# Optimization experiments

Hardware: AMD Instinct MI355X
Metric: run time of the kernel (lower is better)

The kernel has to match this reference:

```python
import jax, jax.numpy as jnp
import numpy as np

EMB = 256
HEADS = 4
HEAD_DIM = EMB // HEADS
N = 4096
M = 4096


def setup_inputs() -> dict:
    key = jax.random.key(0)
    ks = jax.random.split(key, 7)
    s = 1.0 / np.sqrt(EMB)  # keep logits in a sane range
    return {
        "A": jax.random.normal(ks[0], (N, EMB), jnp.float32),
        "B": jax.random.normal(ks[1], (M, EMB), jnp.float32),
        "Wq": jax.random.normal(ks[2], (EMB, EMB), jnp.float32) * s,
        "Wk": jax.random.normal(ks[3], (EMB, EMB), jnp.float32) * s,
        "Wv": jax.random.normal(ks[4], (EMB, EMB), jnp.float32) * s,
        "Wo": jax.random.normal(ks[5], (EMB, EMB), jnp.float32) * s,
        "bo": jnp.zeros((EMB,), jnp.float32),
    }


def _cross_attend(X, Y, Wq, Wk, Wv, Wo, bo):
    # X attends to Y. X:[n,emb], Y:[m,emb]
    scale = jnp.asarray(np.sqrt(HEAD_DIM), X.dtype)
    Q = (X @ Wq.T).reshape(X.shape[0], HEADS, HEAD_DIM)  # [n,h,d]
    K = (Y @ Wk.T).reshape(Y.shape[0], HEADS, HEAD_DIM)  # [m,h,d]
    V = (Y @ Wv.T).reshape(Y.shape[0], HEADS, HEAD_DIM)  # [m,h,d]
    scores = jnp.einsum("nhd,mhd->hnm", Q, K) / scale      # [h,n,m]
    attn = jax.nn.softmax(scores, axis=-1)                   # dropout p=0.0 -> identity
    ctx = jnp.einsum("hnm,mhd->nhd", attn, V).reshape(X.shape[0], EMB)
    return ctx @ Wo.T + bo + X                               # out proj + residual


def reference(A, B, Wq, Wk, Wv, Wo, bo):
    A_out = _cross_attend(A, B, Wq, Wk, Wv, Wo, bo)
    B_out = _cross_attend(B, A, Wq, Wk, Wv, Wo, bo)
    return (A_out, B_out)
```

## Files before the change

### kernel.cpp

```cpp
#include <hip/hip_runtime.h>
#include <hip/hip_bf16.h>
#include <math.h>

#define EMB 256
#define HEADS 4
#define HD 64
#define NTOK 4096

typedef __attribute__((ext_vector_type(8))) short bf16x8;
typedef __attribute__((ext_vector_type(4))) float f32x4;
typedef __attribute__((ext_vector_type(16))) float f32x16;

#define MFMA16(a, b, c) __builtin_amdgcn_mfma_f32_16x16x32_bf16(a, b, c, 0, 0, 0)
#define MFMA32(a, b, c) __builtin_amdgcn_mfma_f32_32x32x16_bf16(a, b, c, 0, 0, 0)

static __device__ __forceinline__ ushort f2bf(float f) {
    __hip_bfloat16 h = __float2bfloat16(f);
    return *(ushort*)&h;
}
static __device__ __forceinline__ float ex2(float x) { return __builtin_amdgcn_exp2f(x); }
static __device__ __forceinline__ uint pkbf(float lo, float hi) {
    uint r;
    asm("v_cvt_pk_bf16_f32 %0, %1, %2" : "=v"(r) : "v"(lo), "v"(hi));
    return r;
}
static __device__ __forceinline__ float max3f(float a, float b, float c) {
    float r;
    asm("v_max3_f32 %0, %1, %2, %3" : "=v"(r) : "v"(a), "v"(b), "v"(c));
    return r;
}
static __device__ __forceinline__ bf16x8 cvt8(float4 a, float4 b) {
    union { uint u[4]; bf16x8 h; } pk;
    pk.u[0] = pkbf(a.x, a.y);
    pk.u[1] = pkbf(a.z, a.w);
    pk.u[2] = pkbf(b.x, b.y);
    pk.u[3] = pkbf(b.z, b.w);
    return pk.h;
}
static __device__ __forceinline__ float bf2f(ushort u) {
    return __uint_as_float(((uint)u) << 16);
}

__global__ void cvtW(const float* __restrict__ Wq, const float* __restrict__ Wk,
                     const float* __restrict__ Wv, const float* __restrict__ Wo,
                     ushort* __restrict__ Wall) {
    const float* s = (blockIdx.y == 0) ? Wq : (blockIdx.y == 1) ? Wk : (blockIdx.y == 2) ? Wv : Wo;
    ushort* d = Wall + (size_t)blockIdx.y * 65536;
    int i = (blockIdx.x * 256 + threadIdx.x) * 4;
    float4 v = *(const float4*)(s + i);
    ushort4 o;
    o.x = f2bf(v.x); o.y = f2bf(v.y); o.z = f2bf(v.z); o.w = f2bf(v.w);
    *(ushort4*)(d + i) = o;
}

__global__ __launch_bounds__(256) void qkv_proj(const float* __restrict__ Xa,
                                                const float* __restrict__ Xb,
                                                const ushort* __restrict__ Wall,
                                                ushort* __restrict__ Q0, ushort* __restrict__ K1, ushort* __restrict__ Vt1,
                                                ushort* __restrict__ Q1, ushort* __restrict__ K0, ushort* __restrict__ Vt0) {
    int w = threadIdx.x >> 6, lane = threadIdx.x & 63;
    int lr = lane & 15, lg = lane >> 4;
    int z = blockIdx.z;
    const float* X = z ? Xb : Xa;
    ushort* Qo = z ? Q1 : Q0;
    ushort* Ko = z ? K0 : K1;
    ushort* Vto = z ? Vt0 : Vt1;
    int rbase = blockIdx.x * 64 + w * 16;
    int cbase = blockIdx.y * 64;

    f32x4 acc[3][4] = {};
#pragma unroll
    for (int kk = 0; kk < 256; kk += 32) {
        const float* xr = X + (size_t)(rbase + lr) * EMB + kk + lg * 8;
        bf16x8 a = cvt8(*(const float4*)xr, *(const float4*)(xr + 4));
#pragma unroll
        for (int kind = 0; kind < 3; ++kind) {
            const ushort* W = Wall + (size_t)kind * 65536;
#pragma unroll
            for (int cj = 0; cj < 4; ++cj) {
                bf16x8 b = *(const bf16x8*)(W + (size_t)(cbase + cj * 16 + lr) * EMB + kk + lg * 8);
                acc[kind][cj] = MFMA16(a, b, acc[kind][cj]);
            }
        }
    }
    const float QS = 0.125f * 1.4426950408889634f;
#pragma unroll
    for (int cj = 0; cj < 4; ++cj)
#pragma unroll
        for (int j = 0; j < 4; ++j) {
            int R = rbase + lg * 4 + j;
            int col = cbase + cj * 16 + lr;
            Qo[(size_t)R * EMB + col] = f2bf(acc[0][cj][j] * QS);
            Ko[(size_t)R * EMB + col] = f2bf(acc[1][cj][j]);
            int h = col >> 6, d = col & 63;
            int Rp = (R & ~12) | ((R & 4) << 1) | ((R & 8) >> 1);
            Vto[(size_t)h * HD * NTOK + (size_t)d * NTOK + Rp] = f2bf(acc[2][cj][j]);
        }
}

__global__ __launch_bounds__(256, 4) void attn(const ushort* __restrict__ Q0,
                                               const ushort* __restrict__ K0,
                                               const ushort* __restrict__ Vt0,
                                               const ushort* __restrict__ Q1,
                                               const ushort* __restrict__ K1,
                                               const ushort* __restrict__ Vt1,
                                               ushort* __restrict__ Opart,
                                               float* __restrict__ ML) {
    __shared__ ushort lK[2][64 * 64];
    __shared__ ushort lV[2][64 * 64];

    int fb = blockIdx.x + 32 * blockIdx.y + 128 * blockIdx.z;
    int nf = (fb & 7) * 128 + (fb >> 3);
    int qt = nf & 31;
    int head = (nf >> 5) & 3;
    int z = nf >> 7;
    int dir = z >> 2, split = z & 3;
    int kv0 = split * 1024;

    const ushort* Q = dir ? Q1 : Q0;
    const ushort* K = dir ? K1 : K0;
    const ushort* Vt = dir ? Vt1 : Vt0;
    const ushort* Vth = Vt + (size_t)head * HD * NTOK;

    int wq = threadIdx.x >> 6;
    int lane = threadIdx.x & 63;
    int l31 = lane & 31, hi = lane >> 5;

    int qg = qt * 128 + wq * 32 + l31;
    bf16x8 qf[4];
#pragma unroll
    for (int ks = 0; ks < 4; ++ks)
        qf[ks] = *(const bf16x8*)(Q + (size_t)qg * EMB + head * 64 + ks * 16 + hi * 8);

    int srow = threadIdx.x >> 3, sseg = threadIdx.x & 7;
    int ssw = (sseg ^ ((srow >> 2) & 7)) * 8;

    uint4 rk0 = *(const uint4*)(K + (size_t)(kv0 + srow) * EMB + head * 64 + sseg * 8);
    uint4 rk1 = *(const uint4*)(K + (size_t)(kv0 + srow + 32) * EMB + head * 64 + sseg * 8);
    uint4 rv0 = *(const uint4*)(Vth + (size_t)srow * NTOK + kv0 + sseg * 8);
    uint4 rv1 = *(const uint4*)(Vth + (size_t)(srow + 32) * NTOK + kv0 + sseg * 8);

    float m = -1e30f, ls = 0.0f;
    f32x16 oacc0 = {};
    f32x16 oacc1 = {};
    int sw = (l31 >> 2) & 7;

    for (int t = 0; t < 16; ++t) {
        int cur = t & 1;
        ushort* lk = &lK[cur][0];
        ushort* lv = &lV[cur][0];
        *(uint4*)(&lk[srow * 64 + ssw]) = rk0;
        *(uint4*)(&lk[(srow + 32) * 64 + ssw]) = rk1;
        *(uint4*)(&lv[srow * 64 + ssw]) = rv0;
        *(uint4*)(&lv[(srow + 32) * 64 + ssw]) = rv1;
        __syncthreads();

        if (t < 15) {
            int nkv = kv0 + (t + 1) * 64;
            rk0 = *(const uint4*)(K + (size_t)(nkv + srow) * EMB + head * 64 + sseg * 8);
            rk1 = *(const uint4*)(K + (size_t)(nkv + srow + 32) * EMB + head * 64 + sseg * 8);
            rv0 = *(const uint4*)(Vth + (size_t)srow * NTOK + nkv + sseg * 8);
            rv1 = *(const uint4*)(Vth + (size_t)(srow + 32) * NTOK + nkv + sseg * 8);
        }

        f32x16 sA = {}, sB = {};
        __builtin_amdgcn_s_setprio(1);
#pragma unroll
        for (int ks = 0; ks < 4; ++ks) {
            bf16x8 ka = *(const bf16x8*)(&lk[l31 * 64 + ((ks * 2 + hi) ^ sw) * 8]);
            bf16x8 kb = *(const bf16x8*)(&lk[(32 + l31) * 64 + ((ks * 2 + hi) ^ sw) * 8]);
            sA = MFMA32(ka, qf[ks], sA);
            sB = MFMA32(kb, qf[ks], sB);
        }
        __builtin_amdgcn_s_setprio(0);

        float t0 = max3f(sA[0], sA[1], sA[2]);
        float t1 = max3f(sA[3], sA[4], sA[5]);
        float t2 = max3f(sA[6], sA[7], sA[8]);
        float t3 = max3f(sA[9], sA[10], sA[11]);
        float t4 = max3f(sA[12], sA[13], sA[14]);
        float t5 = max3f(sB[0], sB[1], sB[2]);
        float t6 = max3f(sB[3], sB[4], sB[5]);
        float t7 = max3f(sB[6], sB[7], sB[8]);
        float t8 = max3f(sB[9], sB[10], sB[11]);
        float t9 = max3f(sB[12], sB[13], sB[14]);
        float ta = fmaxf(sA[15], sB[15]);
        float u0 = max3f(t0, t1, t2);
        float u1 = max3f(t3, t4, t5);
        float u2 = max3f(t6, t7, t8);
        float u3 = fmaxf(t9, ta);
        float tmax = fmaxf(max3f(u0, u1, u2), u3);
        tmax = fmaxf(tmax, __shfl_xor(tmax, 32));

        if (__any(tmax > m + 8.0f)) {
            float mn = fmaxf(m, tmax);
            float sc = ex2(m - mn);
            m = mn;
            ls *= sc;
#pragma unroll
            for (int r = 0; r < 16; ++r) { oacc0[r] *= sc; oacc1[r] *= sc; }
        }

#pragma unroll
        for (int r = 0; r < 16; ++r) sA[r] = ex2(sA[r] - m);
#pragma unroll
        for (int r = 0; r < 16; ++r) sB[r] = ex2(sB[r] - m);

        float s1[16];
#pragma unroll
        for (int i = 0; i < 8; ++i) s1[i] = sA[2 * i] + sA[2 * i + 1];
#pragma unroll
        for (int i = 0; i < 8; ++i) s1[8 + i] = sB[2 * i] + sB[2 * i + 1];
#pragma unroll
        for (int w2 = 8; w2 >= 1; w2 >>= 1)
#pragma unroll
            for (int i = 0; i < 8; ++i)
                if (i < w2) s1[i] = s1[2 * i] + s1[2 * i + 1];
        float rs = s1[0];
        rs += __shfl_xor(rs, 32);
        ls += rs;

        bf16x8 pa[4];
#pragma unroll
        for (int ks = 0; ks < 4; ++ks) {
            union { uint u[4]; bf16x8 h; } pk;
#pragma unroll
            for (int j = 0; j < 4; ++j) {
                float lo = (ks < 2) ? sA[(ks & 1) * 8 + 2 * j] : sB[(ks & 1) * 8 + 2 * j];
                float hv = (ks < 2) ? sA[(ks & 1) * 8 + 2 * j + 1] : sB[(ks & 1) * 8 + 2 * j + 1];
                pk.u[j] = pkbf(lo, hv);
            }
            pa[ks] = pk.h;
        }

        __builtin_amdgcn_s_setprio(1);
#pragma unroll
        for (int ks = 0; ks < 4; ++ks) {
            bf16x8 va = *(const bf16x8*)(&lv[l31 * 64 + ((ks * 2 + hi) ^ sw) * 8]);
            bf16x8 vb = *(const bf16x8*)(&lv[(32 + l31) * 64 + ((ks * 2 + hi) ^ sw) * 8]);
            oacc0 = MFMA32(va, pa[ks], oacc0);
            oacc1 = MFMA32(vb, pa[ks], oacc1);
        }
        __builtin_amdgcn_s_setprio(0);
    }

    ushort* Ob = Opart + ((size_t)z * 4096 + qg) * 256 + head * 64;
#pragma unroll
    for (int r = 0; r < 16; ++r) {
        int crow = (r & 3) + 8 * (r >> 2) + 4 * hi;
        Ob[crow] = f2bf(oacc0[r]);
        Ob[32 + crow] = f2bf(oacc1[r]);
    }
    if (hi == 0) {
        float2* mlp = (float2*)ML;
        mlp[((size_t)z * 4 + head) * 4096 + qg] = make_float2(m, ls);
    }
}

__global__ __launch_bounds__(256) void merge(const ushort* __restrict__ Opart,
                                             const float* __restrict__ ML,
                                             ushort* __restrict__ C0,
                                             ushort* __restrict__ C1) {
    int idx = blockIdx.x * 256 + threadIdx.x;
    int dblk = idx & 7;
    int head = (idx >> 3) & 3;
    int q = (idx >> 5) & 4095;
    int dir = idx >> 17;

    const float2* mlp = (const float2*)ML;
    float2 ml[4];
    float M = -1e30f;
#pragma unroll
    for (int s = 0; s < 4; ++s) {
        ml[s] = mlp[((size_t)(dir * 4 + s) * 4 + head) * 4096 + q];
        M = fmaxf(M, ml[s].x);
    }
    float denom = 0.0f, a[4];
#pragma unroll
    for (int s = 0; s < 4; ++s) { a[s] = ex2(ml[s].x - M); denom += a[s] * ml[s].y; }
    float inv = 1.0f / denom;

    float accv[8] = {};
#pragma unroll
    for (int s = 0; s < 4; ++s) {
        float ws = a[s] * inv;
        bf16x8 x = *(const bf16x8*)(Opart + ((size_t)(dir * 4 + s) * 4096 + q) * 256 + head * 64 + dblk * 8);
#pragma unroll
        for (int u = 0; u < 8; ++u) accv[u] += ws * bf2f((ushort)x[u]);
    }
    float4 c0 = {accv[0], accv[1], accv[2], accv[3]};
    float4 c1 = {accv[4], accv[5], accv[6], accv[7]};
    ushort* C = (dir ? C1 : C0) + (size_t)q * 256 + head * 64 + dblk * 8;
    *(bf16x8*)C = cvt8(c0, c1);
}

__global__ __launch_bounds__(256) void out_proj(const ushort* __restrict__ C0,
                                                const ushort* __restrict__ C1,
                                                const ushort* __restrict__ Wo,
                                                const float* __restrict__ bo,
                                                const float* __restrict__ A,
                                                const float* __restrict__ B,
                                                float* __restrict__ out) {
    int dir = blockIdx.z;
    const ushort* Ctx = dir ? C1 : C0;
    const float* X = dir ? B : A;
    float* o = out + (size_t)dir * NTOK * EMB;

    int w = threadIdx.x >> 6, lane = threadIdx.x & 63;
    int lr = lane & 15, lg = lane >> 4;
    int rbase = blockIdx.x * 64 + w * 16;
    int cbase = blockIdx.y * 64;

    f32x4 acc[4] = {};
#pragma unroll
    for (int kk = 0; kk < 256; kk += 32) {
        bf16x8 a = *(const bf16x8*)(Ctx + (size_t)(rbase + lr) * EMB + kk + lg * 8);
#pragma unroll
        for (int cj = 0; cj < 4; ++cj) {
            bf16x8 b = *(const bf16x8*)(Wo + (size_t)(cbase + cj * 16 + lr) * EMB + kk + lg * 8);
            acc[cj] = MFMA16(a, b, acc[cj]);
        }
    }
#pragma unroll
    for (int cj = 0; cj < 4; ++cj)
#pragma unroll
        for (int j = 0; j < 4; ++j) {
            int R = rbase + lg * 4 + j;
            int col = cbase + cj * 16 + lr;
            o[(size_t)R * EMB + col] = acc[cj][j] + bo[col] + X[(size_t)R * EMB + col];
        }
}

extern "C" void kernel_launch(void* const* d_in, const int* in_sizes, int n_in,
                              void* d_out, int out_size, void* d_ws, size_t ws_size,
                              hipStream_t stream) {
    const float* A  = (const float*)d_in[0];
    const float* B  = (const float*)d_in[1];
    const float* Wq = (const float*)d_in[2];
    const float* Wk = (const float*)d_in[3];
    const float* Wv = (const float*)d_in[4];
    const float* Wo = (const float*)d_in[5];
    const float* bo = (const float*)d_in[6];
    float* out = (float*)d_out;

    ushort* ws = (ushort*)d_ws;
    const size_t TE = (size_t)NTOK * EMB;
    ushort* wall = ws;
    ushort* q0  = wall + 4 * 65536;
    ushort* q1  = q0 + TE;
    ushort* k0  = q1 + TE;
    ushort* k1  = k0 + TE;
    ushort* vt0 = k1 + TE;
    ushort* vt1 = vt0 + TE;
    ushort* c0  = vt1 + TE;
    ushort* c1  = c0 + TE;
    ushort* Opart = c1 + TE;
    float* ML = (float*)(Opart + (size_t)8 * 4096 * 256);

    cvtW<<<dim3(64, 4), 256, 0, stream>>>(Wq, Wk, Wv, Wo, wall);

    qkv_proj<<<dim3(64, 4, 2), 256, 0, stream>>>(A, B, wall, q0, k1, vt1, q1, k0, vt0);

    attn<<<dim3(32, 4, 8), 256, 0, stream>>>(q0, k0, vt0, q1, k1, vt1, Opart, ML);

    merge<<<dim3(1024), 256, 0, stream>>>(Opart, ML, c0, c1);

    out_proj<<<dim3(64, 4, 2), 256, 0, stream>>>(c0, c1, wall + 3 * 65536, bo, A, B, out);
}
```

Measured before the change: 105.8 us.

## Pre-convert inputs to bf16, split QKV projection per kind, use permlane32 reductions

Adds a kernel that converts A and B to bf16 once. The QKV projection grid grows from 2 to 6 z-slices, so each block computes one of Q, K or V, giving three times the blocks and fewer accumulator registers. In the attention kernel, the cross-half max and sum reductions use permlane32_swap in place of __shfl_xor. The cost is an extra launch plus a bf16 round trip for the inputs, and each block re-reads its X tile once per kind.

```diff
diff --git a/kernel.cpp b/kernel.cpp
--- a/kernel.cpp
+++ b/kernel.cpp
@@ -10,6 +10,7 @@
 typedef __attribute__((ext_vector_type(8))) short bf16x8;
 typedef __attribute__((ext_vector_type(4))) float f32x4;
 typedef __attribute__((ext_vector_type(16))) float f32x16;
+typedef __attribute__((ext_vector_type(2))) unsigned int uint2v;
 
 #define MFMA16(a, b, c) __builtin_amdgcn_mfma_f32_16x16x32_bf16(a, b, c, 0, 0, 0)
 #define MFMA32(a, b, c) __builtin_amdgcn_mfma_f32_32x32x16_bf16(a, b, c, 0, 0, 0)
@@ -28,6 +29,16 @@
     float r;
     asm("v_max3_f32 %0, %1, %2, %3" : "=v"(r) : "v"(a), "v"(b), "v"(c));
     return r;
+}
+static __device__ __forceinline__ float redmax32(float x) {
+    uint xi = __float_as_uint(x);
+    uint2v r = __builtin_amdgcn_permlane32_swap(xi, xi, false, false);
+    return fmaxf(__uint_as_float(r[0]), __uint_as_float(r[1]));
+}
+static __device__ __forceinline__ float redsum32(float x) {
+    uint xi = __float_as_uint(x);
+    uint2v r = __builtin_amdgcn_permlane32_swap(xi, xi, false, false);
+    return __uint_as_float(r[0]) + __uint_as_float(r[1]);
 }
 static __device__ __forceinline__ bf16x8 cvt8(float4 a, float4 b) {
     union { uint u[4]; bf16x8 h; } pk;
@@ -39,6 +50,17 @@
 }
 static __device__ __forceinline__ float bf2f(ushort u) {
     return __uint_as_float(((uint)u) << 16);
+}
+
+__global__ void cvtAB(const float* __restrict__ A, const float* __restrict__ B,
+                      ushort* __restrict__ Ao, ushort* __restrict__ Bo) {
+    const float* s = blockIdx.y ? B : A;
+    ushort* d = blockIdx.y ? Bo : Ao;
+    int i = (blockIdx.x * 256 + threadIdx.x) * 4;
+    float4 v = *(const float4*)(s + i);
+    ushort4 o;
+    o.x = f2bf(v.x); o.y = f2bf(v.y); o.z = f2bf(v.z); o.w = f2bf(v.w);
+    *(ushort4*)(d + i) = o;
 }
 
 __global__ void cvtW(const float* __restrict__ Wq, const float* __restrict__ Wk,
@@ -53,34 +75,31 @@
     *(ushort4*)(d + i) = o;
 }
 
-__global__ __launch_bounds__(256) void qkv_proj(const float* __restrict__ Xa,
-                                                const float* __restrict__ Xb,
+__global__ __launch_bounds__(256) void qkv_proj(const ushort* __restrict__ Xa,
+                                                const ushort* __restrict__ Xb,
                                                 const ushort* __restrict__ Wall,
                                                 ushort* __restrict__ Q0, ushort* __restrict__ K1, ushort* __restrict__ Vt1,
                                                 ushort* __restrict__ Q1, ushort* __restrict__ K0, ushort* __restrict__ Vt0) {
     int w = threadIdx.x >> 6, lane = threadIdx.x & 63;
     int lr = lane & 15, lg = lane >> 4;
     int z = blockIdx.z;
-    const float* X = z ? Xb : Xa;
-    ushort* Qo = z ? Q1 : Q0;
-    ushort* Ko = z ? K0 : K1;
-    ushort* Vto = z ? Vt0 : Vt1;
+    int kind = (z < 3) ? z : z - 3;
+    const ushort* X = (z < 3) ? Xa : Xb;
+    ushort* Qo = (z < 3) ? Q0 : Q1;
+    ushort* Ko = (z < 3) ? K1 : K0;
+    ushort* Vto = (z < 3) ? Vt1 : Vt0;
+    const ushort* W = Wall + (size_t)kind * 65536;
     int rbase = blockIdx.x * 64 + w * 16;
     int cbase = blockIdx.y * 64;
 
-    f32x4 acc[3][4] = {};
+    f32x4 acc[4] = {};
 #pragma unroll
     for (int kk = 0; kk < 256; kk += 32) {
-        const float* xr = X + (size_t)(rbase + lr) * EMB + kk + lg * 8;
-        bf16x8 a = cvt8(*(const float4*)xr, *(const float4*)(xr + 4));
-#pragma unroll
-        for (int kind = 0; kind < 3; ++kind) {
-            const ushort* W = Wall + (size_t)kind * 65536;
-#pragma unroll
-            for (int cj = 0; cj < 4; ++cj) {
-                bf16x8 b = *(const bf16x8*)(W + (size_t)(cbase + cj * 16 + lr) * EMB + kk + lg * 8);
-                acc[kind][cj] = MFMA16(a, b, acc[kind][cj]);
-            }
+        bf16x8 a = *(const bf16x8*)(X + (size_t)(rbase + lr) * EMB + kk + lg * 8);
+#pragma unroll
+        for (int cj = 0; cj < 4; ++cj) {
+            bf16x8 b = *(const bf16x8*)(W + (size_t)(cbase + cj * 16 + lr) * EMB + kk + lg * 8);
+            acc[cj] = MFMA16(a, b, acc[cj]);
         }
     }
     const float QS = 0.125f * 1.4426950408889634f;
@@ -90,11 +109,16 @@
         for (int j = 0; j < 4; ++j) {
             int R = rbase + lg * 4 + j;
             int col = cbase + cj * 16 + lr;
-            Qo[(size_t)R * EMB + col] = f2bf(acc[0][cj][j] * QS);
-            Ko[(size_t)R * EMB + col] = f2bf(acc[1][cj][j]);
-            int h = col >> 6, d = col & 63;
-            int Rp = (R & ~12) | ((R & 4) << 1) | ((R & 8) >> 1);
-            Vto[(size_t)h * HD * NTOK + (size_t)d * NTOK + Rp] = f2bf(acc[2][cj][j]);
+            float v = acc[cj][j];
+            if (kind == 0) {
+                Qo[(size_t)R * EMB + col] = f2bf(v * QS);
+            } else if (kind == 1) {
+                Ko[(size_t)R * EMB + col] = f2bf(v);
+            } else {
+                int h = col >> 6, d = col & 63;
+                int Rp = (R & ~12) | ((R & 4) << 1) | ((R & 8) >> 1);
+                Vto[(size_t)h * HD * NTOK + (size_t)d * NTOK + Rp] = f2bf(v);
+            }
         }
 }
 
@@ -189,8 +213,7 @@
         float u1 = max3f(t3, t4, t5);
         float u2 = max3f(t6, t7, t8);
         float u3 = fmaxf(t9, ta);
-        float tmax = fmaxf(max3f(u0, u1, u2), u3);
-        tmax = fmaxf(tmax, __shfl_xor(tmax, 32));
+        float tmax = redmax32(fmaxf(max3f(u0, u1, u2), u3));
 
         if (__any(tmax > m + 8.0f)) {
             float mn = fmaxf(m, tmax);
@@ -216,9 +239,7 @@
 #pragma unroll
             for (int i = 0; i < 8; ++i)
                 if (i < w2) s1[i] = s1[2 * i] + s1[2 * i + 1];
-        float rs = s1[0];
-        rs += __shfl_xor(rs, 32);
-        ls += rs;
+        ls += redsum32(s1[0]);
 
         bf16x8 pa[4];
 #pragma unroll
@@ -346,7 +367,9 @@
     ushort* ws = (ushort*)d_ws;
     const size_t TE = (size_t)NTOK * EMB;
     ushort* wall = ws;
-    ushort* q0  = wall + 4 * 65536;
+    ushort* abf = wall + 4 * 65536;
+    ushort* bbf = abf + TE;
+    ushort* q0  = bbf + TE;
     ushort* q1  = q0 + TE;
     ushort* k0  = q1 + TE;
     ushort* k1  = k0 + TE;
@@ -357,9 +380,10 @@
     ushort* Opart = c1 + TE;
     float* ML = (float*)(Opart + (size_t)8 * 4096 * 256);
 
+    cvtAB<<<dim3(1024, 2), 256, 0, stream>>>(A, B, abf, bbf);
     cvtW<<<dim3(64, 4), 256, 0, stream>>>(Wq, Wk, Wv, Wo, wall);
 
-    qkv_proj<<<dim3(64, 4, 2), 256, 0, stream>>>(A, B, wall, q0, k1, vt1, q1, k0, vt0);
+    qkv_proj<<<dim3(64, 4, 6), 256, 0, stream>>>(abf, bbf, wall, q0, k1, vt1, q1, k0, vt0);
 
     attn<<<dim3(32, 4, 8), 256, 0, stream>>>(q0, k0, vt0, q1, k1, vt1, Opart, ML);
 
```

After: 106.9 us. About the same (+1.0%).
